# Optimization experiments

Measured on AMD Instinct MI355X. Metric: run time of the kernel, lower is better.

The kernel has to match this reference:

```python
import jax, jax.numpy as jnp
import numpy as np

FEATURE_DIM = 3
INPUT_DIM = FEATURE_DIM + 1
HIDDEN = 64


def setup_inputs() -> dict:
    key = jax.random.key(0)
    k_f, k1, k2, k3 = jax.random.split(key, 4)
    N, T = 262144, 60
    features = jax.random.normal(k_f, (N, T, FEATURE_DIM), dtype=jnp.float32)
    # PyTorch nn.Linear default init: U(-1/sqrt(fan_in), 1/sqrt(fan_in))
    def linear(k, fin, fout):
        ka, kb = jax.random.split(k)
        bound = 1.0 / np.sqrt(fin)
        W = jax.random.uniform(ka, (fin, fout), jnp.float32, -bound, bound)
        b = jax.random.uniform(kb, (fout,), jnp.float32, -bound, bound)
        return W, b
    W1, b1 = linear(k1, INPUT_DIM, HIDDEN)
    W2, b2 = linear(k2, HIDDEN, HIDDEN)
    W3, b3 = linear(k3, HIDDEN, 1)
    return {"features": features, "W1": W1, "b1": b1, "W2": W2, "b2": b2,
            "W3": W3, "b3": b3}


def reference(features, W1, b1, W2, b2, W3, b3):
    # features: (N, T, F). Sequential unroll over T with delta feedback.
    N, T, F = features.shape
    feats_t = jnp.swapaxes(features, 0, 1)  # (T, N, F)

    def step(delta_prev, f_t):
        # x_t: (N, INPUT_DIM) = [features_t, delta_{t-1}]
        x = jnp.concatenate([f_t, delta_prev[:, None]], axis=-1)
        h = jax.nn.relu(x @ W1 + b1)
        h = jax.nn.relu(h @ W2 + b2)
        delta = (h @ W3 + b3)[:, 0]  # (N,)
        return delta, delta

    delta0 = jnp.zeros((N,), dtype=features.dtype)
    _, deltas = jax.lax.scan(step, delta0, feats_t)  # (T, N)
    return jnp.swapaxes(deltas, 0, 1)  # (N, T)
```

## Files before the change

### kernel.cpp

```cpp
#include <hip/hip_runtime.h>
#include <hip/hip_bf16.h>

#define TSTEPS 60
#define HIDDEN 64

typedef __attribute__((ext_vector_type(8))) short bf16x8;
typedef __attribute__((ext_vector_type(4))) float f32x4;

__device__ __forceinline__ short f2bf(float f) {
    return __builtin_bit_cast(short, __float2bfloat16(f));
}

__global__ __launch_bounds__(256)
void ffn_mfma(const float* __restrict__ feat,
              const float* __restrict__ W1, const float* __restrict__ b1,
              const float* __restrict__ W2, const float* __restrict__ b2,
              const float* __restrict__ W3, const float* __restrict__ b3,
              float* __restrict__ out, int N) {
    __shared__ short h1s[4][1024];
    __shared__ float dlt[4][16 * TSTEPS];

    const int lane = threadIdx.x & 63;
    const int wave = threadIdx.x >> 6;
    const int c = lane & 15;
    const int g = lane >> 4;
    const int nbase = blockIdx.x * 64 + wave * 16;
    if (nbase >= N) return;

    bf16x8 a1[4];
#pragma unroll
    for (int m = 0; m < 4; ++m) {
        bf16x8 v = {0, 0, 0, 0, 0, 0, 0, 0};
        if (g == 0) {
#pragma unroll
            for (int j = 0; j < 4; ++j) v[j] = f2bf(W1[j * 64 + m * 16 + c]);
        }
        a1[m] = v;
    }
    bf16x8 a2[4][2];
#pragma unroll
    for (int m = 0; m < 4; ++m)
#pragma unroll
        for (int q = 0; q < 2; ++q) {
            bf16x8 v;
#pragma unroll
            for (int j = 0; j < 8; ++j)
                v[j] = f2bf(W2[(32 * q + 8 * g + j) * 64 + m * 16 + c]);
            a2[m][q] = v;
        }
    f32x4 b1f[4], b2f[4], w3f[4];
#pragma unroll
    for (int m = 0; m < 4; ++m)
#pragma unroll
        for (int r = 0; r < 4; ++r) {
            b1f[m][r] = b1[m * 16 + 4 * g + r];
            b2f[m][r] = b2[m * 16 + 4 * g + r];
            w3f[m][r] = W3[m * 16 + 4 * g + r];
        }
    const float b3v = b3[0];

    char* hbase = (char*)&h1s[wave][0];
    const int swz = (c & 7) << 4;
    int woff[4], roff[2];
#pragma unroll
    for (int m = 0; m < 4; ++m) woff[m] = (c * 128 + m * 32 + g * 8) ^ swz;
#pragma unroll
    for (int q = 0; q < 2; ++q) roff[q] = (c * 128 + q * 64 + g * 16) ^ swz;

    const float* fp = feat + (size_t)(nbase + c) * (TSTEPS * 3);
    float f0 = fp[0], f1 = fp[1], f2 = fp[2];
    float nf0 = 0.f, nf1 = 0.f, nf2 = 0.f;
    float delta = 0.0f;

    for (int t = 0; t < TSTEPS; ++t) {
        if (t + 1 < TSTEPS) {
            nf0 = fp[t * 3 + 3]; nf1 = fp[t * 3 + 4]; nf2 = fp[t * 3 + 5];
        }

        bf16x8 xb;
        xb[0] = f2bf(f0); xb[1] = f2bf(f1); xb[2] = f2bf(f2); xb[3] = f2bf(delta);
        xb[4] = 0; xb[5] = 0; xb[6] = 0; xb[7] = 0;

        f32x4 h1a[4];
#pragma unroll
        for (int m = 0; m < 4; ++m)
            h1a[m] = __builtin_amdgcn_mfma_f32_16x16x32_bf16(a1[m], xb, b1f[m], 0, 0, 0);

#pragma unroll
        for (int m = 0; m < 4; ++m) {
            unsigned lo = ((unsigned)(unsigned short)f2bf(fmaxf(h1a[m][1], 0.f)) << 16)
                        | (unsigned short)f2bf(fmaxf(h1a[m][0], 0.f));
            unsigned hi = ((unsigned)(unsigned short)f2bf(fmaxf(h1a[m][3], 0.f)) << 16)
                        | (unsigned short)f2bf(fmaxf(h1a[m][2], 0.f));
            uint2 u; u.x = lo; u.y = hi;
            *(uint2*)(hbase + woff[m]) = u;
        }
        __asm__ volatile("" ::: "memory");

        bf16x8 hb0 = *(const bf16x8*)(hbase + roff[0]);
        bf16x8 hb1 = *(const bf16x8*)(hbase + roff[1]);

        f32x4 acc[4];
#pragma unroll
        for (int m = 0; m < 4; ++m) {
            acc[m] = __builtin_amdgcn_mfma_f32_16x16x32_bf16(a2[m][0], hb0, b2f[m], 0, 0, 0);
            acc[m] = __builtin_amdgcn_mfma_f32_16x16x32_bf16(a2[m][1], hb1, acc[m], 0, 0, 0);
        }

        float p = 0.f;
#pragma unroll
        for (int m = 0; m < 4; ++m)
#pragma unroll
            for (int r = 0; r < 4; ++r)
                p = fmaf(fmaxf(acc[m][r], 0.f), w3f[m][r], p);
        p += __shfl_xor(p, 16, 64);
        p += __shfl_xor(p, 32, 64);
        delta = p + b3v;

        if (g == 0) dlt[wave][c * TSTEPS + t] = delta;
        f0 = nf0; f1 = nf1; f2 = nf2;
    }

    float* ob = out + (size_t)nbase * TSTEPS;
#pragma unroll 1
    for (int i = lane; i < 16 * TSTEPS; i += 64) ob[i] = dlt[wave][i];
}

extern "C" void kernel_launch(void* const* d_in, const int* in_sizes, int n_in,
                              void* d_out, int out_size, void* d_ws, size_t ws_size,
                              hipStream_t stream) {
    const float* feat = (const float*)d_in[0];
    const float* W1   = (const float*)d_in[1];
    const float* b1   = (const float*)d_in[2];
    const float* W2   = (const float*)d_in[3];
    const float* b2   = (const float*)d_in[4];
    const float* W3   = (const float*)d_in[5];
    const float* b3   = (const float*)d_in[6];
    float* out = (float*)d_out;

    const int N = in_sizes[0] / (TSTEPS * 3);
    const int block = 256;
    const int grid = (N + 63) / 64;
    ffn_mfma<<<grid, block, 0, stream>>>(feat, W1, b1, W2, b2, W3, b3, out, N);
}
```

Measured before the change: 294.1 us.

## Write outputs directly in float4 chunks, unroll timesteps by four, cheaper bf16 pack

Removes the LDS staging buffer for the per-row outputs and has lanes with g==0 store four consecutive timestep results as one 16-byte global write. The time loop is unrolled by four, and feature loads are issued inside each step rather than through an explicit one-step register prefetch. Float-to-bf16 conversion becomes an integer add-and-shift that rounds half away from zero instead of the library's round-to-nearest-even. This frees LDS and shortens the conversion path, but the global stores are now scattered across rows and feature-load latency is left to the scheduler.

```diff
diff --git a/kernel.cpp b/kernel.cpp
--- a/kernel.cpp
+++ b/kernel.cpp
@@ -11,6 +11,12 @@
     return __builtin_bit_cast(short, __float2bfloat16(f));
 }
 
+__device__ __forceinline__ unsigned pack2_bf16(float a, float b) {
+    unsigned ua = __builtin_bit_cast(unsigned, a) + 0x8000u;
+    unsigned ub = __builtin_bit_cast(unsigned, b) + 0x8000u;
+    return (ua >> 16) | (ub & 0xFFFF0000u);
+}
+
 __global__ __launch_bounds__(256)
 void ffn_mfma(const float* __restrict__ feat,
               const float* __restrict__ W1, const float* __restrict__ b1,
@@ -18,7 +24,6 @@
               const float* __restrict__ W3, const float* __restrict__ b3,
               float* __restrict__ out, int N) {
     __shared__ short h1s[4][1024];
-    __shared__ float dlt[4][16 * TSTEPS];
 
     const int lane = threadIdx.x & 63;
     const int wave = threadIdx.x >> 6;
@@ -68,18 +73,19 @@
     for (int q = 0; q < 2; ++q) roff[q] = (c * 128 + q * 64 + g * 16) ^ swz;
 
     const float* fp = feat + (size_t)(nbase + c) * (TSTEPS * 3);
-    float f0 = fp[0], f1 = fp[1], f2 = fp[2];
-    float nf0 = 0.f, nf1 = 0.f, nf2 = 0.f;
+    float* o = out + (size_t)(nbase + c) * TSTEPS;
     float delta = 0.0f;
 
-    for (int t = 0; t < TSTEPS; ++t) {
-        if (t + 1 < TSTEPS) {
-            nf0 = fp[t * 3 + 3]; nf1 = fp[t * 3 + 4]; nf2 = fp[t * 3 + 5];
-        }
+    auto step = [&](int t) -> float {
+        const float f0 = fp[t * 3 + 0];
+        const float f1 = fp[t * 3 + 1];
+        const float f2 = fp[t * 3 + 2];
 
-        bf16x8 xb;
-        xb[0] = f2bf(f0); xb[1] = f2bf(f1); xb[2] = f2bf(f2); xb[3] = f2bf(delta);
-        xb[4] = 0; xb[5] = 0; xb[6] = 0; xb[7] = 0;
+        uint4 xu;
+        xu.x = pack2_bf16(f0, f1);
+        xu.y = pack2_bf16(f2, delta);
+        xu.z = 0u; xu.w = 0u;
+        const bf16x8 xb = __builtin_bit_cast(bf16x8, xu);
 
         f32x4 h1a[4];
 #pragma unroll
@@ -88,17 +94,16 @@
 
 #pragma unroll
         for (int m = 0; m < 4; ++m) {
-            unsigned lo = ((unsigned)(unsigned short)f2bf(fmaxf(h1a[m][1], 0.f)) << 16)
-                        | (unsigned short)f2bf(fmaxf(h1a[m][0], 0.f));
-            unsigned hi = ((unsigned)(unsigned short)f2bf(fmaxf(h1a[m][3], 0.f)) << 16)
-                        | (unsigned short)f2bf(fmaxf(h1a[m][2], 0.f));
-            uint2 u; u.x = lo; u.y = hi;
+            uint2 u;
+            u.x = pack2_bf16(fmaxf(h1a[m][0], 0.f), fmaxf(h1a[m][1], 0.f));
+            u.y = pack2_bf16(fmaxf(h1a[m][2], 0.f), fmaxf(h1a[m][3], 0.f));
             *(uint2*)(hbase + woff[m]) = u;
         }
         __asm__ volatile("" ::: "memory");
 
-        bf16x8 hb0 = *(const bf16x8*)(hbase + roff[0]);
-        bf16x8 hb1 = *(const bf16x8*)(hbase + roff[1]);
+        const bf16x8 hb0 = *(const bf16x8*)(hbase + roff[0]);
+        const bf16x8 hb1 = *(const bf16x8*)(hbase + roff[1]);
+        __asm__ volatile("" ::: "memory");
 
         f32x4 acc[4];
 #pragma unroll
@@ -115,15 +120,19 @@
                 p = fmaf(fmaxf(acc[m][r], 0.f), w3f[m][r], p);
         p += __shfl_xor(p, 16, 64);
         p += __shfl_xor(p, 32, 64);
-        delta = p + b3v;
+        return p + b3v;
+    };
 
-        if (g == 0) dlt[wave][c * TSTEPS + t] = delta;
-        f0 = nf0; f1 = nf1; f2 = nf2;
+    for (int tb = 0; tb < TSTEPS; tb += 4) {
+        const float d0 = step(tb + 0); delta = d0;
+        const float d1 = step(tb + 1); delta = d1;
+        const float d2 = step(tb + 2); delta = d2;
+        const float d3 = step(tb + 3); delta = d3;
+        if (g == 0) {
+            f32x4 v = {d0, d1, d2, d3};
+            *(f32x4*)(o + tb) = v;
+        }
     }
-
-    float* ob = out + (size_t)nbase * TSTEPS;
-#pragma unroll 1
-    for (int i = lane; i < 16 * TSTEPS; i += 64) ob[i] = dlt[wave][i];
 }
 
 extern "C" void kernel_launch(void* const* d_in, const int* in_sizes, int n_in,
```

Measured after the change: 319.5 us. +8.6%, slower.
